# Optimization experiments

Hardware: AMD Instinct MI355X
Metric: run time of the kernel (lower is better)

## Reference

```python
import jax, jax.numpy as jnp
import numpy as np

N, K, P, D, H = 1024, 32, 1024, 512, 256
FDIM = 3 * P + 3 * D + 4  # 4612
GLOBAL_MEAN_AFFINITY = 6.5


def _init_linear(key, fan_in, fan_out):
    kw, kb = jax.random.split(key)
    bound = 1.0 / np.sqrt(fan_in)
    w = jax.random.uniform(kw, (fan_in, fan_out), jnp.float32, -bound, bound)
    b = jax.random.uniform(kb, (fan_out,), jnp.float32, -bound, bound)
    return w, b


def setup_inputs() -> dict:
    key = jax.random.key(0)
    ks = jax.random.split(key, 16)
    inp = {
        "neighbor_protein": jax.random.normal(ks[0], (N, K, P), jnp.float32),
        "neighbor_drug": jax.random.normal(ks[1], (N, K, D), jnp.float32),
        "neighbor_affinity": jax.random.normal(ks[2], (N, K), jnp.float32),
        "neighbor_ppr": jax.random.uniform(ks[3], (N, K), jnp.float32),
        "neighbor_trust": jax.random.uniform(ks[4], (N, K), jnp.float32),
        "neighbor_mask": jax.random.randint(ks[5], (N, K), 0, 2).astype(bool),
        "qry_protein": jax.random.normal(ks[6], (N, P), jnp.float32),
        "qry_drug": jax.random.normal(ks[7], (N, D), jnp.float32),
    }
    # weight_net params
    inp["w1"], inp["wb1"] = _init_linear(ks[8], FDIM, H)
    inp["w2"], inp["wb2"] = _init_linear(ks[9], H, H // 2)
    inp["w3"], inp["wb3"] = _init_linear(ks[10], H // 2, 1)
    # delta_net params
    inp["d1"], inp["db1"] = _init_linear(ks[11], FDIM, H)
    inp["d2"], inp["db2"] = _init_linear(ks[12], H, H // 2)
    inp["d3"], inp["db3"] = _init_linear(ks[13], H // 2, 1)
    # binding_encoder params (MLP over [qry_protein, qry_drug])
    inp["be1"], inp["beb1"] = _init_linear(ks[14], P + D, H)
    inp["be2"], inp["beb2"] = _init_linear(ks[15], H, 1)
    inp["log_sigma"] = jnp.zeros((1,), jnp.float32)
    return inp


def _mlp3(x, w1, b1, w2, b2, w3, b3):
    h = jax.nn.relu(x @ w1 + b1)
    h = jax.nn.relu(h @ w2 + b2)
    return (h @ w3 + b3)[..., 0]


def _cosine_sim(a, b, eps=1e-8):
    na = jnp.maximum(jnp.linalg.norm(a, axis=-1), eps)
    nb = jnp.maximum(jnp.linalg.norm(b, axis=-1), eps)
    return jnp.sum(a * b, axis=-1) / (na * nb)


def reference(neighbor_protein, neighbor_drug, neighbor_affinity, neighbor_ppr,
              neighbor_trust, neighbor_mask, qry_protein, qry_drug,
              w1, wb1, w2, wb2, w3, wb3,
              d1, db1, d2, db2, d3, db3,
              be1, beb1, be2, beb2, log_sigma):
    # --- feature build: [N, K, FDIM] ---
    qp = jnp.broadcast_to(qry_protein[:, None, :], neighbor_protein.shape)
    qd = jnp.broadcast_to(qry_drug[:, None, :], neighbor_drug.shape)
    drug_sim = _cosine_sim(qd, neighbor_drug)  # [N, K]
    features = jnp.concatenate([
        qp, neighbor_protein, qp - neighbor_protein,
        qd, neighbor_drug, qd - neighbor_drug,
        neighbor_affinity[..., None], neighbor_ppr[..., None],
        neighbor_trust[..., None], drug_sim[..., None],
    ], axis=-1)

    # --- weight net + masked softmax over K ---
    logits = _mlp3(features, w1, wb1, w2, wb2, w3, wb3)  # [N, K]
    logits = jnp.where(neighbor_mask, logits, -1e9)
    weights = jax.nn.softmax(logits, axis=1) * neighbor_mask.astype(jnp.float32)
    norm = jnp.sum(weights, axis=1, keepdims=True)
    weights = jnp.where(norm > 0, weights / jnp.maximum(norm, 1e-8),
                        jnp.zeros_like(weights))

    transfer = jnp.sum(weights * neighbor_affinity, axis=1)  # [N]
    delta = _mlp3(features, d1, db1, d2, db2, d3, db3)  # [N, K]
    correction = jnp.sum(weights * delta, axis=1)  # [N]

    # --- binding encoder prior ---
    be_in = jnp.concatenate([qry_protein, qry_drug], axis=-1)
    prior = (jax.nn.relu(be_in @ be1 + beb1) @ be2 + beb2)[..., 0] + GLOBAL_MEAN_AFFINITY

    has_neighbors = jnp.any(neighbor_mask, axis=1)  # [N]
    mu = jnp.where(has_neighbors, transfer + correction, prior)
    base_sigma = jnp.broadcast_to(jax.nn.softplus(log_sigma), mu.shape)
    sigma = base_sigma + (~has_neighbors).astype(jnp.float32) * 0.15 + 1e-4
    return mu, sigma
```

## Files before the change

### kernel.cpp

```cpp
#include <hip/hip_runtime.h>
#include <cstdint>
#include <cstddef>


typedef __attribute__((ext_vector_type(8))) short s16x8;
typedef __attribute__((ext_vector_type(4))) float f32x4;

static __device__ __forceinline__ unsigned short f2bf(float f) {
  unsigned u = __float_as_uint(f);
  u += 0x7fffu + ((u >> 16) & 1u);
  return (unsigned short)(u >> 16);
}

static __device__ __forceinline__ void glds16(const void* g, void* l) {
  __builtin_amdgcn_global_load_lds(
      (const __attribute__((address_space(1))) void*)g,
      (__attribute__((address_space(3))) void*)l, 16, 0, 0);
}

__global__ void prep_k(const float* __restrict__ qp, const float* __restrict__ qd,
                       unsigned short* __restrict__ Aq, float* __restrict__ qn,
                       const float* __restrict__ w1, const float* __restrict__ d1,
                       const float* __restrict__ be1, const float* __restrict__ w2,
                       const float* __restrict__ d2,
                       unsigned short* __restrict__ Bt1,
                       unsigned short* __restrict__ Btq,
                       unsigned short* __restrict__ Bt2c) {
  const int t = threadIdx.x;
  if (blockIdx.x < 1024) {
    const int n = blockIdx.x;
    const float4* qp4 = (const float4*)(qp + (size_t)n * 1024);
    float4 v = qp4[t];
    ushort4 o4;
    o4.x = f2bf(v.x); o4.y = f2bf(v.y); o4.z = f2bf(v.z); o4.w = f2bf(v.w);
    *(ushort4*)(Aq + (size_t)n * 1536 + t * 4) = o4;
    const float2* qd2 = (const float2*)(qd + (size_t)n * 512);
    float2 w = qd2[t];
    ushort2 o2; o2.x = f2bf(w.x); o2.y = f2bf(w.y);
    *(ushort2*)(Aq + (size_t)n * 1536 + 1024 + t * 2) = o2;
    float ss = w.x * w.x + w.y * w.y;
    #pragma unroll
    for (int m = 32; m >= 1; m >>= 1) ss += __shfl_xor(ss, m);
    __shared__ float sr[4];
    if ((t & 63) == 0) sr[t >> 6] = ss;
    __syncthreads();
    if (t == 0) qn[n] = sqrtf(sr[0] + sr[1] + sr[2] + sr[3]);
    return;
  }
  const int NB1 = 512 * 1536, NBQ = 768 * 1536, NB2 = 256 * 256;
  const int nb = gridDim.x - 1024;
  for (int idx = (blockIdx.x - 1024) * 256 + t; idx < NB1 + NBQ + NB2;
       idx += nb * 256) {
    if (idx < NB1) {
      int c = idx / 1536, j = idx - c * 1536;
      const float* W = (c < 256) ? w1 : d1;
      int cc = c & 255;
      float v;
      if (j < 1024) v = W[(1024 + j) * 256 + cc] - W[(2048 + j) * 256 + cc];
      else { int jd = j - 1024; v = W[(3584 + jd) * 256 + cc] - W[(4096 + jd) * 256 + cc]; }
      Bt1[idx] = f2bf(v);
    } else if (idx < NB1 + NBQ) {
      int i2 = idx - NB1;
      int c = i2 / 1536, j = i2 - c * 1536;
      float v;
      if (c < 512) {
        const float* W = (c < 256) ? w1 : d1;
        int cc = c & 255;
        if (j < 1024) v = W[j * 256 + cc] + W[(2048 + j) * 256 + cc];
        else { int jd = j - 1024; v = W[(3072 + jd) * 256 + cc] + W[(4096 + jd) * 256 + cc]; }
      } else {
        v = be1[j * 256 + (c - 512)];
      }
      Btq[i2] = f2bf(v);
    } else {
      int i2 = idx - NB1 - NBQ;
      int o = i2 >> 8, j = i2 & 255;
      float v = (o < 128) ? w2[j * 128 + o] : d2[j * 128 + (o - 128)];
      Bt2c[i2] = f2bf(v);
    }
  }
}

__global__ __launch_bounds__(256) void gemm0_k(
    const unsigned short* __restrict__ abf, const unsigned short* __restrict__ Bt,
    const float* __restrict__ wb1, const float* __restrict__ db1,
    const float* __restrict__ beb1, float* __restrict__ uq_out) {
  __shared__ short As[64 * 64];
  __shared__ short Bs[64 * 64];
  const int tid = threadIdx.x;
  const int l = tid & 63, w = tid >> 6;
  const int br = blockIdx.x, bc = blockIdx.y;
  const int c0 = bc * 64;
  const int lc = l & 15, lk = l >> 4;
  f32x4 acc[4] = {};

  for (int kt = 0; kt < 24; ++kt) {
    const int k0 = kt * 64;
    __syncthreads();
    #pragma unroll
    for (int i = 0; i < 2; ++i) {
      int q = i * 256 + tid;
      int row = q >> 3, slot = q & 7;
      int sw = (slot ^ (row & 7)) * 8;
      glds16(abf + (size_t)(br * 64 + row) * 1536 + k0 + sw, &As[q * 8]);
      glds16(Bt + (size_t)(c0 + row) * 1536 + k0 + sw, &Bs[q * 8]);
    }
    __syncthreads();
    #pragma unroll
    for (int kh = 0; kh < 2; ++kh) {
      int ra = w * 16 + lc;
      int sla = (kh * 4 + lk) ^ (ra & 7);
      s16x8 af = *(const s16x8*)(&As[ra * 64 + sla * 8]);
      #pragma unroll
      for (int ni = 0; ni < 4; ++ni) {
        int rb = ni * 16 + lc;
        int slb = (kh * 4 + lk) ^ (rb & 7);
        s16x8 bf = *(const s16x8*)(&Bs[rb * 64 + slb * 8]);
        acc[ni] = __builtin_amdgcn_mfma_f32_16x16x32_bf16(af, bf, acc[ni], 0, 0, 0);
      }
    }
  }
  #pragma unroll
  for (int ni = 0; ni < 4; ++ni)
    #pragma unroll
    for (int r = 0; r < 4; ++r) {
      int rowl = w * 16 + lk * 4 + r;
      int gcol = c0 + ni * 16 + lc;
      long grow = (long)br * 64 + rowl;
      float b = (gcol < 256) ? wb1[gcol]
               : (gcol < 512) ? db1[gcol - 256] : beb1[gcol - 512];
      uq_out[grow * 768 + gcol] = acc[ni][r] + b;
    }
}

__global__ __launch_bounds__(512, 2) void gemm1_k(
    const float* __restrict__ Anp, const float* __restrict__ And,
    const unsigned short* __restrict__ Bt,
    const float* __restrict__ uq, const float* __restrict__ aff,
    const float* __restrict__ ppr, const float* __restrict__ trs,
    const float* __restrict__ qd, const float* __restrict__ qn,
    const float* __restrict__ w1, const float* __restrict__ d1,
    const unsigned short* __restrict__ Bt2c,
    const float* __restrict__ wb2, const float* __restrict__ db2,
    const float* __restrict__ w3, const float* __restrict__ wb3,
    const float* __restrict__ d3, const float* __restrict__ db3,
    const int* __restrict__ msk, const float* __restrict__ be2,
    const float* __restrict__ beb2, const float* __restrict__ lsg,
    float* __restrict__ out) {
  __shared__ short As[2][128 * 64];
  __shared__ short Bs[2][512 * 64];
  const int tid = threadIdx.x;
  const int l = tid & 63, w = tid >> 6;
  const int wr = w >> 2, wc = w & 3;
  const long br = blockIdx.x;
  const int arow = tid >> 2, aseg = tid & 3;
  const long agrow = br * 128 + arow;
  const long an = agrow >> 5;
  const int brow = tid >> 3, bslot = tid & 7;
  const int lc = l & 15, lk = l >> 4;

  f32x4 acc[4][8] = {};
  float areg[16], qreg[16];
  float dotp = 0.f, nsp = 0.f;

  auto stageBhalf = [&](int buf, int kt, int h) {
    const int k0 = kt * 64;
    #pragma unroll
    for (int i = 0; i < 4; ++i) {
      int idx = h * 4 + i;
      int row = idx * 64 + brow;
      const unsigned short* src =
          Bt + (size_t)row * 1536 + k0 + ((bslot ^ (row & 7)) * 8);
      glds16(src, &Bs[buf][(idx * 512 + tid) * 8]);
    }
  };
  auto loadA = [&](int kt) {
    const int k0 = kt * 64 + aseg * 16;
    const float* src = (k0 < 1024) ? (Anp + agrow * 1024 + k0)
                                   : (And + agrow * 512 + (k0 - 1024));
    #pragma unroll
    for (int i = 0; i < 4; ++i) {
      float4 v = ((const float4*)src)[i];
      areg[i * 4 + 0] = v.x; areg[i * 4 + 1] = v.y;
      areg[i * 4 + 2] = v.z; areg[i * 4 + 3] = v.w;
    }
    if (kt >= 16) {
      const float* qs = qd + an * 512 + (k0 - 1024);
      #pragma unroll
      for (int i = 0; i < 4; ++i) {
        float4 v = ((const float4*)qs)[i];
        qreg[i * 4 + 0] = v.x; qreg[i * 4 + 1] = v.y;
        qreg[i * 4 + 2] = v.z; qreg[i * 4 + 3] = v.w;
      }
    }
  };
  auto writeA = [&](int buf, int kt) {
    if (kt >= 16) {
      #pragma unroll
      for (int j = 0; j < 16; ++j) {
        dotp += areg[j] * qreg[j];
        nsp  += areg[j] * areg[j];
      }
    }
    #pragma unroll
    for (int j = 0; j < 2; ++j) {
      int slot = (aseg * 2 + j) ^ (arow & 7);
      s16x8 pk;
      #pragma unroll
      for (int e = 0; e < 8; ++e) pk[e] = (short)f2bf(areg[j * 8 + e]);
      *(s16x8*)(&As[buf][arow * 64 + slot * 8]) = pk;
    }
  };

  auto rdA = [&](int cur, int kh, s16x8* af) {
    #pragma unroll
    for (int mi = 0; mi < 4; ++mi) {
      int ra = wr * 64 + mi * 16 + lc;
      int sl = (kh * 4 + lk) ^ (ra & 7);
      af[mi] = *(const s16x8*)(&As[cur][ra * 64 + sl * 8]);
    }
  };
  auto rdB = [&](int cur, int kh, int nh, s16x8* bfr) {
    #pragma unroll
    for (int ni = 0; ni < 4; ++ni) {
      int rb = wc * 128 + (nh * 4 + ni) * 16 + lc;
      int sl = (kh * 4 + lk) ^ (rb & 7);
      bfr[ni] = *(const s16x8*)(&Bs[cur][rb * 64 + sl * 8]);
    }
  };

  loadA(0);
  stageBhalf(0, 0, 0); stageBhalf(0, 0, 1);
  writeA(0, 0);
  __syncthreads();

  for (int kt = 0; kt < 24; ++kt) {
    const int cur = kt & 1, nxt = cur ^ 1;
    if (kt < 23) {
      loadA(kt + 1);
      asm volatile("s_waitcnt vmcnt(4)" ::: "memory");
    } else {
      asm volatile("s_waitcnt vmcnt(0)" ::: "memory");
    }
    asm volatile("s_waitcnt lgkmcnt(0)" ::: "memory");
    __builtin_amdgcn_s_barrier();
    __builtin_amdgcn_sched_barrier(0);

    s16x8 af[4], bfr[4];
    rdA(cur, 0, af); rdB(cur, 0, 0, bfr);
    asm volatile("s_waitcnt lgkmcnt(0)" ::: "memory");
    __builtin_amdgcn_sched_barrier(0);
    __builtin_amdgcn_s_setprio(1);
    #pragma unroll
    for (int mi = 0; mi < 4; ++mi)
      #pragma unroll
      for (int ni = 0; ni < 4; ++ni)
        acc[mi][ni] = __builtin_amdgcn_mfma_f32_16x16x32_bf16(
            af[mi], bfr[ni], acc[mi][ni], 0, 0, 0);
    __builtin_amdgcn_s_setprio(0);
    if (kt < 23) stageBhalf(nxt, kt + 1, 0);
    rdB(cur, 0, 1, bfr);
    asm volatile("s_waitcnt lgkmcnt(0)" ::: "memory");
    __builtin_amdgcn_sched_barrier(0);
    __builtin_amdgcn_s_setprio(1);
    #pragma unroll
    for (int mi = 0; mi < 4; ++mi)
      #pragma unroll
      for (int ni = 0; ni < 4; ++ni)
        acc[mi][4 + ni] = __builtin_amdgcn_mfma_f32_16x16x32_bf16(
            af[mi], bfr[ni], acc[mi][4 + ni], 0, 0, 0);
    __builtin_amdgcn_s_setprio(0);
    if (kt < 23) stageBhalf(nxt, kt + 1, 1);
    rdA(cur, 1, af); rdB(cur, 1, 0, bfr);
    asm volatile("s_waitcnt lgkmcnt(0)" ::: "memory");
    __builtin_amdgcn_sched_barrier(0);
    __builtin_amdgcn_s_setprio(1);
    #pragma unroll
    for (int mi = 0; mi < 4; ++mi)
      #pragma unroll
      for (int ni = 0; ni < 4; ++ni)
        acc[mi][ni] = __builtin_amdgcn_mfma_f32_16x16x32_bf16(
            af[mi], bfr[ni], acc[mi][ni], 0, 0, 0);
    __builtin_amdgcn_s_setprio(0);
    if (kt < 23) writeA(nxt, kt + 1);
    rdB(cur, 1, 1, bfr);
    asm volatile("s_waitcnt lgkmcnt(0)" ::: "memory");
    __builtin_amdgcn_sched_barrier(0);
    __builtin_amdgcn_s_setprio(1);
    #pragma unroll
    for (int mi = 0; mi < 4; ++mi)
      #pragma unroll
      for (int ni = 0; ni < 4; ++ni)
        acc[mi][4 + ni] = __builtin_amdgcn_mfma_f32_16x16x32_bf16(
            af[mi], bfr[ni], acc[mi][4 + ni], 0, 0, 0);
    __builtin_amdgcn_s_setprio(0);
  }

  float* simLds = (float*)&As[0][0];
  float dv = dotp, nv = nsp;
  dv += __shfl_xor(dv, 1); dv += __shfl_xor(dv, 2);
  nv += __shfl_xor(nv, 1); nv += __shfl_xor(nv, 2);
  __syncthreads();
  if (aseg == 0) {
    float qv = qn[an];
    simLds[arow] = dv / (fmaxf(qv, 1e-8f) * fmaxf(sqrtf(nv), 1e-8f));
  }
  __syncthreads();

  short* h1l = &Bs[0][0];
  #pragma unroll
  for (int mi = 0; mi < 4; ++mi) {
    #pragma unroll
    for (int r = 0; r < 4; ++r) {
      int rowl = wr * 64 + mi * 16 + lk * 4 + r;
      long grow = br * 128 + rowl;
      float sa = aff[grow], sp = ppr[grow], st = trs[grow];
      float ss = simLds[rowl];
      long n = grow >> 5;
      #pragma unroll
      for (int ni = 0; ni < 8; ++ni) {
        int gcol = wc * 128 + ni * 16 + lc;
        const float* W = (gcol < 256) ? w1 : d1;
        int cc2 = gcol & 255;
        float sv = sa * W[4608 * 256 + cc2] + sp * W[4609 * 256 + cc2]
                 + st * W[4610 * 256 + cc2] + ss * W[4611 * 256 + cc2];
        float x = acc[mi][ni][r] + uq[n * 768 + gcol] + sv;
        int chsw = (gcol >> 3) ^ (rowl & 7);
        h1l[rowl * 512 + chsw * 8 + (gcol & 7)] = (short)f2bf(fmaxf(x, 0.f));
      }
    }
  }
  __syncthreads();

  short* B2 = &As[0][0];
  f32x4 acc2[4][4] = {};
  const int rh = w >> 2;
  const int oq = w & 3;
  const int ob = oq * 64;
  const int kbase = (oq < 2) ? 0 : 256;
  for (int cc = 0; cc < 4; ++cc) {
    #pragma unroll
    for (int i = 0; i < 4; ++i) {
      int q = i * 512 + tid;
      int o = q >> 3, sl = q & 7;
      const unsigned short* src =
          Bt2c + (size_t)o * 256 + cc * 64 + ((sl ^ (o & 7)) * 8);
      glds16(src, &B2[q * 8]);
    }
    __syncthreads();
    #pragma unroll
    for (int kh = 0; kh < 2; ++kh) {
      s16x8 a2[4], b2f[4];
      #pragma unroll
      for (int mi = 0; mi < 4; ++mi) {
        int row = rh * 64 + mi * 16 + lc;
        int acol = kbase + cc * 64 + kh * 32 + lk * 8;
        int chsw = (acol >> 3) ^ (row & 7);
        a2[mi] = *(const s16x8*)(&h1l[row * 512 + chsw * 8]);
      }
      #pragma unroll
      for (int ni = 0; ni < 4; ++ni) {
        int o = ob + ni * 16 + lc;
        int sl = (kh * 4 + lk) ^ (o & 7);
        b2f[ni] = *(const s16x8*)(&B2[o * 64 + sl * 8]);
      }
      #pragma unroll
      for (int mi = 0; mi < 4; ++mi)
        #pragma unroll
        for (int ni = 0; ni < 4; ++ni)
          acc2[mi][ni] = __builtin_amdgcn_mfma_f32_16x16x32_bf16(
              a2[mi], b2f[ni], acc2[mi][ni], 0, 0, 0);
    }
    __syncthreads();
  }

  float coef[4], bb[4];
  #pragma unroll
  for (int ni = 0; ni < 4; ++ni) {
    int o = ob + ni * 16 + lc;
    coef[ni] = (o < 128) ? w3[o] : d3[o - 128];
    bb[ni]   = (o < 128) ? wb2[o] : db2[o - 128];
  }
  float* part = (float*)&As[0][0];
  #pragma unroll
  for (int mi = 0; mi < 4; ++mi) {
    #pragma unroll
    for (int rr = 0; rr < 4; ++rr) {
      float p = 0.f;
      #pragma unroll
      for (int ni = 0; ni < 4; ++ni)
        p += fmaxf(acc2[mi][ni][rr] + bb[ni], 0.f) * coef[ni];
      p += __shfl_xor(p, 1); p += __shfl_xor(p, 2);
      p += __shfl_xor(p, 4); p += __shfl_xor(p, 8);
      if (lc == 0)
        part[oq * 128 + rh * 64 + mi * 16 + lk * 4 + rr] = p;
    }
  }
  __syncthreads();

  if (w < 2) {
    const int half = l >> 5, kk = l & 31;
    const int rowl = (w * 2 + half) * 32 + kk;
    const long n = br * 4 + w * 2 + half;
    float lgt = part[0 * 128 + rowl] + part[1 * 128 + rowl] + wb3[0];
    float dlt = part[2 * 128 + rowl] + part[3 * 128 + rowl] + db3[0];
    float pp = 0.f;
    const float* uqr = uq + (size_t)n * 768 + 512 + kk * 8;
    #pragma unroll
    for (int j = 0; j < 8; ++j)
      pp += fmaxf(uqr[j], 0.f) * be2[kk * 8 + j];
    #pragma unroll
    for (int mm = 16; mm >= 1; mm >>= 1) pp += __shfl_xor(pp, mm);
    int m = msk[n * 32 + kk];
    float lg = m ? lgt : -1e9f;
    float mx = lg;
    #pragma unroll
    for (int mm = 16; mm >= 1; mm >>= 1) mx = fmaxf(mx, __shfl_xor(mx, mm));
    float e = expf(lg - mx);
    float s = e;
    #pragma unroll
    for (int mm = 16; mm >= 1; mm >>= 1) s += __shfl_xor(s, mm);
    float wgt = (e / s) * (m ? 1.f : 0.f);
    float nrm = wgt;
    #pragma unroll
    for (int mm = 16; mm >= 1; mm >>= 1) nrm += __shfl_xor(nrm, mm);
    wgt = (nrm > 0.f) ? wgt / fmaxf(nrm, 1e-8f) : 0.f;
    float tr = wgt * aff[n * 32 + kk];
    float co = wgt * dlt;
    int am = m;
    #pragma unroll
    for (int mm = 16; mm >= 1; mm >>= 1) {
      tr += __shfl_xor(tr, mm);
      co += __shfl_xor(co, mm);
      am |= __shfl_xor(am, mm);
    }
    if (kk == 0) {
      float prior = pp + beb2[0] + 6.5f;
      float l0 = lsg[0];
      float sp = (l0 > 20.f) ? l0 : log1pf(expf(l0));
      out[n] = am ? (tr + co) : prior;
      out[1024 + n] = sp + (am ? 0.f : 0.15f) + 1e-4f;
    }
  }
}

extern "C" void kernel_launch(void* const* d_in, const int* in_sizes, int n_in,
                              void* d_out, int out_size, void* d_ws, size_t ws_size,
                              hipStream_t stream) {
  const float* np_ = (const float*)d_in[0];
  const float* nd_ = (const float*)d_in[1];
  const float* aff = (const float*)d_in[2];
  const float* ppr = (const float*)d_in[3];
  const float* trs = (const float*)d_in[4];
  const int*   msk = (const int*)d_in[5];
  const float* qp  = (const float*)d_in[6];
  const float* qd  = (const float*)d_in[7];
  const float* w1  = (const float*)d_in[8];
  const float* wb1 = (const float*)d_in[9];
  const float* w2  = (const float*)d_in[10];
  const float* wb2 = (const float*)d_in[11];
  const float* w3  = (const float*)d_in[12];
  const float* wb3 = (const float*)d_in[13];
  const float* d1  = (const float*)d_in[14];
  const float* db1 = (const float*)d_in[15];
  const float* d2  = (const float*)d_in[16];
  const float* db2 = (const float*)d_in[17];
  const float* d3  = (const float*)d_in[18];
  const float* db3 = (const float*)d_in[19];
  const float* be1 = (const float*)d_in[20];
  const float* beb1 = (const float*)d_in[21];
  const float* be2 = (const float*)d_in[22];
  const float* beb2 = (const float*)d_in[23];
  const float* lsg = (const float*)d_in[24];
  float* out = (float*)d_out;

  char* ws = (char*)d_ws;
  size_t off = 0;
  auto carve = [&](size_t bytes) -> void* {
    void* p = ws + off;
    off += (bytes + 511) & ~(size_t)511;
    return p;
  };
  float*          uq   = (float*)carve(1024ull * 768 * 4);
  unsigned short* Bt1  = (unsigned short*)carve(512ull * 1536 * 2);
  unsigned short* Btq  = (unsigned short*)carve(768ull * 1536 * 2);
  unsigned short* Bt2c = (unsigned short*)carve(256ull * 256 * 2);
  unsigned short* Aq   = (unsigned short*)carve(1024ull * 1536 * 2);
  float*          qn   = (float*)carve(1024ull * 4);
  (void)ws_size; (void)in_sizes; (void)n_in; (void)out_size;

  prep_k<<<3072, 256, 0, stream>>>(qp, qd, Aq, qn,
                                   w1, d1, be1, w2, d2, Bt1, Btq, Bt2c);

  gemm0_k<<<dim3(16, 12), 256, 0, stream>>>(Aq, Btq, wb1, db1, beb1, uq);

  gemm1_k<<<256, 512, 0, stream>>>(np_, nd_, Bt1, uq, aff, ppr, trs,
                                   qd, qn, w1, d1,
                                   Bt2c, wb2, db2, w3, wb3, d3, db3,
                                   msk, be2, beb2, lsg, out);
}
```

Baseline: 124.3 us.

## Replace hand-scheduled MFMA main loop with simple staged loop and syncthreads

Swaps the hand-interleaved K-loop for a plain structure. The old loop split B staging into halves issued between MFMA groups, with explicit waitcnt, sched_barrier and setprio hints. The new loop issues all next-tile B and A global loads up front, then runs two k-halves of 4x8 MFMAs, writes A, and ends each iteration with __syncthreads. This leaves instruction scheduling to the compiler and simplifies synchronisation. The cost is losing the fine-grained overlap of LDS reads and global-to-LDS staging with MFMA work, and a full barrier is added every iteration.

```diff
diff --git a/kernel.cpp b/kernel.cpp
--- a/kernel.cpp
+++ b/kernel.cpp
@@ -163,15 +163,14 @@
   float areg[16], qreg[16];
   float dotp = 0.f, nsp = 0.f;
 
-  auto stageBhalf = [&](int buf, int kt, int h) {
+  auto stageB = [&](int buf, int kt) {
     const int k0 = kt * 64;
     #pragma unroll
-    for (int i = 0; i < 4; ++i) {
-      int idx = h * 4 + i;
-      int row = idx * 64 + brow;
+    for (int i = 0; i < 8; ++i) {
+      int row = i * 64 + brow;
       const unsigned short* src =
           Bt + (size_t)row * 1536 + k0 + ((bslot ^ (row & 7)) * 8);
-      glds16(src, &Bs[buf][(idx * 512 + tid) * 8]);
+      glds16(src, &Bs[buf][(i * 512 + tid) * 8]);
     }
   };
   auto loadA = [&](int kt) {
@@ -212,88 +211,38 @@
     }
   };
 
-  auto rdA = [&](int cur, int kh, s16x8* af) {
-    #pragma unroll
-    for (int mi = 0; mi < 4; ++mi) {
-      int ra = wr * 64 + mi * 16 + lc;
-      int sl = (kh * 4 + lk) ^ (ra & 7);
-      af[mi] = *(const s16x8*)(&As[cur][ra * 64 + sl * 8]);
-    }
-  };
-  auto rdB = [&](int cur, int kh, int nh, s16x8* bfr) {
-    #pragma unroll
-    for (int ni = 0; ni < 4; ++ni) {
-      int rb = wc * 128 + (nh * 4 + ni) * 16 + lc;
-      int sl = (kh * 4 + lk) ^ (rb & 7);
-      bfr[ni] = *(const s16x8*)(&Bs[cur][rb * 64 + sl * 8]);
-    }
-  };
-
+  stageB(0, 0);
   loadA(0);
-  stageBhalf(0, 0, 0); stageBhalf(0, 0, 1);
   writeA(0, 0);
   __syncthreads();
 
   for (int kt = 0; kt < 24; ++kt) {
     const int cur = kt & 1, nxt = cur ^ 1;
-    if (kt < 23) {
-      loadA(kt + 1);
-      asm volatile("s_waitcnt vmcnt(4)" ::: "memory");
-    } else {
-      asm volatile("s_waitcnt vmcnt(0)" ::: "memory");
-    }
-    asm volatile("s_waitcnt lgkmcnt(0)" ::: "memory");
-    __builtin_amdgcn_s_barrier();
-    __builtin_amdgcn_sched_barrier(0);
-
-    s16x8 af[4], bfr[4];
-    rdA(cur, 0, af); rdB(cur, 0, 0, bfr);
-    asm volatile("s_waitcnt lgkmcnt(0)" ::: "memory");
-    __builtin_amdgcn_sched_barrier(0);
-    __builtin_amdgcn_s_setprio(1);
-    #pragma unroll
-    for (int mi = 0; mi < 4; ++mi)
-      #pragma unroll
-      for (int ni = 0; ni < 4; ++ni)
-        acc[mi][ni] = __builtin_amdgcn_mfma_f32_16x16x32_bf16(
-            af[mi], bfr[ni], acc[mi][ni], 0, 0, 0);
-    __builtin_amdgcn_s_setprio(0);
-    if (kt < 23) stageBhalf(nxt, kt + 1, 0);
-    rdB(cur, 0, 1, bfr);
-    asm volatile("s_waitcnt lgkmcnt(0)" ::: "memory");
-    __builtin_amdgcn_sched_barrier(0);
-    __builtin_amdgcn_s_setprio(1);
-    #pragma unroll
-    for (int mi = 0; mi < 4; ++mi)
-      #pragma unroll
-      for (int ni = 0; ni < 4; ++ni)
-        acc[mi][4 + ni] = __builtin_amdgcn_mfma_f32_16x16x32_bf16(
-            af[mi], bfr[ni], acc[mi][4 + ni], 0, 0, 0);
-    __builtin_amdgcn_s_setprio(0);
-    if (kt < 23) stageBhalf(nxt, kt + 1, 1);
-    rdA(cur, 1, af); rdB(cur, 1, 0, bfr);
-    asm volatile("s_waitcnt lgkmcnt(0)" ::: "memory");
-    __builtin_amdgcn_sched_barrier(0);
-    __builtin_amdgcn_s_setprio(1);
-    #pragma unroll
-    for (int mi = 0; mi < 4; ++mi)
-      #pragma unroll
-      for (int ni = 0; ni < 4; ++ni)
-        acc[mi][ni] = __builtin_amdgcn_mfma_f32_16x16x32_bf16(
-            af[mi], bfr[ni], acc[mi][ni], 0, 0, 0);
-    __builtin_amdgcn_s_setprio(0);
+    if (kt < 23) { stageB(nxt, kt + 1); loadA(kt + 1); }
+    #pragma unroll
+    for (int kh = 0; kh < 2; ++kh) {
+      s16x8 af[4], bfr[8];
+      #pragma unroll
+      for (int mi = 0; mi < 4; ++mi) {
+        int ra = wr * 64 + mi * 16 + lc;
+        int sl = (kh * 4 + lk) ^ (ra & 7);
+        af[mi] = *(const s16x8*)(&As[cur][ra * 64 + sl * 8]);
+      }
+      #pragma unroll
+      for (int ni = 0; ni < 8; ++ni) {
+        int rb = wc * 128 + ni * 16 + lc;
+        int sl = (kh * 4 + lk) ^ (rb & 7);
+        bfr[ni] = *(const s16x8*)(&Bs[cur][rb * 64 + sl * 8]);
+      }
+      #pragma unroll
+      for (int mi = 0; mi < 4; ++mi)
+        #pragma unroll
+        for (int ni = 0; ni < 8; ++ni)
+          acc[mi][ni] = __builtin_amdgcn_mfma_f32_16x16x32_bf16(
+              af[mi], bfr[ni], acc[mi][ni], 0, 0, 0);
+    }
     if (kt < 23) writeA(nxt, kt + 1);
-    rdB(cur, 1, 1, bfr);
-    asm volatile("s_waitcnt lgkmcnt(0)" ::: "memory");
-    __builtin_amdgcn_sched_barrier(0);
-    __builtin_amdgcn_s_setprio(1);
-    #pragma unroll
-    for (int mi = 0; mi < 4; ++mi)
-      #pragma unroll
-      for (int ni = 0; ni < 4; ++ni)
-        acc[mi][4 + ni] = __builtin_amdgcn_mfma_f32_16x16x32_bf16(
-            af[mi], bfr[ni], acc[mi][4 + ni], 0, 0, 0);
-    __builtin_amdgcn_s_setprio(0);
+    __syncthreads();
   }
 
   float* simLds = (float*)&As[0][0];
```

New measurement: 130.7 us. 1.05x slower.
